# Performance work log

Hardware: AMD Instinct MI355X
Metric: run time of the kernel (lower is better)

## Reference

```python
import jax, jax.numpy as jnp
import numpy as np

D_MODEL = 128
N_HEADS = 8
N_POINTS = 8
MAX_RES = 10.0


def setup_inputs() -> dict:
    key = jax.random.key(0)
    ks = jax.random.split(key, 12)
    B, C, H, W = 4, D_MODEL, 128, 128
    nh, P = N_HEADS, N_POINTS
    inp = {
        'nbr_fea': jax.random.normal(ks[0], (B, C, H, W), jnp.float32),
        'ext_fea': jax.random.normal(ks[1], (B, C, H, W), jnp.float32),
        'flow': jax.random.normal(ks[2], (B, 2, H, W), jnp.float32) * 2.0,
        'W_off': jax.random.normal(ks[3], (C, nh * P * 2), jnp.float32) * 0.02,
        'b_off': jax.random.normal(ks[4], (nh * P * 2,), jnp.float32) * 0.02,
        'W_attn': jax.random.normal(ks[5], (C, nh * P), jnp.float32) * 0.02,
        'b_attn': jnp.zeros((nh * P,), jnp.float32),
        'W_val': jax.random.normal(ks[6], (C, C), jnp.float32) * (1.0 / np.sqrt(C)),
        'b_val': jnp.zeros((C,), jnp.float32),
        'W_out': jax.random.normal(ks[7], (C, C), jnp.float32) * (1.0 / np.sqrt(C)),
        'b_out': jnp.zeros((C,), jnp.float32),
    }
    return inp


def _bilinear_gather(value, loc, H, W):
    # value: (B, nh, HW, dh)  loc: (B, nh, Q, P, 2) normalized to [0,1]
    # grid_sample semantics: align_corners=False, zero padding
    B, nh, HW, dh = value.shape
    Q, P = loc.shape[2], loc.shape[3]
    x = loc[..., 0] * W - 0.5  # (B,nh,Q,P) pixel coords
    y = loc[..., 1] * H - 0.5
    x0 = jnp.floor(x)
    y0 = jnp.floor(y)
    wx = x - x0
    wy = y - y0
    out = jnp.zeros((B, nh, Q * P, dh), value.dtype)
    for dx, dy, wgt in ((0, 0, (1 - wx) * (1 - wy)), (1, 0, wx * (1 - wy)),
                        (0, 1, (1 - wx) * wy), (1, 1, wx * wy)):
        xi = x0 + dx
        yi = y0 + dy
        valid = (xi >= 0) & (xi < W) & (yi >= 0) & (yi < H)
        xi_c = jnp.clip(xi, 0, W - 1).astype(jnp.int32)
        yi_c = jnp.clip(yi, 0, H - 1).astype(jnp.int32)
        idx = (yi_c * W + xi_c).reshape(B, nh, Q * P, 1)
        g = jnp.take_along_axis(value, idx, axis=2)  # (B,nh,QP,dh)
        w_eff = (wgt * valid.astype(value.dtype)).reshape(B, nh, Q * P, 1)
        out = out + g * w_eff
    return out.reshape(B, nh, Q, P, dh)


def reference(nbr_fea, ext_fea, flow, W_off, b_off, W_attn, b_attn, W_val, b_val, W_out, b_out):
    B, C, H, W = nbr_fea.shape
    nh, P = N_HEADS, N_POINTS
    dh = C // nh
    Q = H * W
    # normalized reference points (pixel centers / extent)
    ys = (jnp.arange(H, dtype=jnp.float32) + 0.5) / H
    xs = (jnp.arange(W, dtype=jnp.float32) + 0.5) / W
    yy, xx = jnp.meshgrid(ys, xs, indexing='ij')
    ref = jnp.stack([xx, yy], -1).reshape(Q, 2)  # (Q,2)

    ext = ext_fea.transpose(0, 2, 3, 1).reshape(B, Q, C)
    # flow-guided sampling offsets (pixels), residue bounded by tanh
    off = MAX_RES * jnp.tanh(ext @ W_off + b_off)
    off = off.reshape(B, Q, nh, P, 2)
    flow_q = flow.transpose(0, 2, 3, 1).reshape(B, Q, 1, 1, 2)
    norm = jnp.array([W, H], jnp.float32)
    loc = ref[None, :, None, None, :] + (flow_q + off) / norm  # (B,Q,nh,P,2)

    attn = jax.nn.softmax((ext @ W_attn + b_attn).reshape(B, Q, nh, P), axis=-1)

    val = (nbr_fea.transpose(0, 2, 3, 1).reshape(B, Q, C) @ W_val + b_val)
    val = val.reshape(B, Q, nh, dh).transpose(0, 2, 1, 3)  # (B,nh,HW,dh)

    sampled = _bilinear_gather(val, loc.transpose(0, 2, 1, 3, 4), H, W)  # (B,nh,Q,P,dh)
    agg = jnp.einsum('bnqpd,bqnp->bqnd', sampled, attn).reshape(B, Q, C)
    out = agg @ W_out + b_out  # (B,Q,C)
    return out.reshape(B, H, W, C).transpose(0, 3, 1, 2)
```

## Files before the change

kernel.cpp:

```cpp
#include <hip/hip_runtime.h>
#include <math.h>

namespace {
constexpr int B   = 4;
constexpr int C   = 128;
constexpr int H   = 128;
constexpr int W   = 128;
constexpr int HWn = H * W;
constexpr int NH  = 8;
}

using short8 = __attribute__((ext_vector_type(8))) short;
using f32x4  = __attribute__((ext_vector_type(4))) float;

__device__ __forceinline__ float fast_tanh(float x) {
  float e = __expf(2.f * x);
  return 1.f - 2.f / (e + 1.f);
}
__device__ __forceinline__ unsigned f2bf(float f) {
  unsigned u = __float_as_uint(f);
  return (u + 0x7FFFu + ((u >> 16) & 1u)) >> 16;
}
__device__ __forceinline__ unsigned pack2bf(float a, float b) {
  return f2bf(a) | (f2bf(b) << 16);
}

__global__ __launch_bounds__(256) void prep_weights_kernel(
    const float* __restrict__ Woff, const float* __restrict__ Wattn,
    const float* __restrict__ Wval, const float* __restrict__ Wout,
    unsigned short* __restrict__ wcat_t, unsigned short* __restrict__ wval_t,
    unsigned short* __restrict__ wout_t) {
  int row = blockIdx.x * 256 + threadIdx.x;
  if (row >= 448) return;
  const float* src; int ldn; int col; unsigned short* dst;
  if (row < 192) {
    if (row < 128) { src = Woff; ldn = 128; col = row; }
    else           { src = Wattn; ldn = 64; col = row - 128; }
    dst = wcat_t + row * 128;
  } else if (row < 320) {
    src = Wval; ldn = 128; col = row - 192; dst = wval_t + (row - 192) * 128;
  } else {
    src = Wout; ldn = 128; col = row - 320; dst = wout_t + (row - 320) * 128;
  }
  for (int k0 = 0; k0 < 128; k0 += 8) {
    unsigned pk[4];
#pragma unroll
    for (int j = 0; j < 4; ++j)
      pk[j] = pack2bf(src[(k0 + 2 * j) * ldn + col],
                      src[(k0 + 2 * j + 1) * ldn + col]);
    *(uint4*)(dst + k0) = make_uint4(pk[0], pk[1], pk[2], pk[3]);
  }
}

__global__ __launch_bounds__(256) void val_gemm_kernel(
    const float* __restrict__ nbr, const unsigned short* __restrict__ wval_t,
    const float* __restrict__ bv, unsigned short* __restrict__ val) {
  __shared__ unsigned short a_s[64 * 152];
  __shared__ unsigned short b_s[128 * 40];
  const int t    = threadIdx.x;
  const int b    = blockIdx.x >> 8;
  const int q0   = (blockIdx.x & 255) * 64;
  const int wv   = t >> 6;
  const int lane = t & 63;
  const int li   = lane & 15, quad = lane >> 4;

  const float* Ab = nbr + (size_t)b * C * HWn + q0;
#pragma unroll
  for (int it = 0; it < 4; ++it) {
    int idx = t + 256 * it;
    int kp  = idx >> 4;
    int q4  = (idx & 15) * 4;
    float4 fa = *(const float4*)(Ab + (size_t)(2 * kp) * HWn + q4);
    float4 fb = *(const float4*)(Ab + (size_t)(2 * kp + 1) * HWn + q4);
    const float* pa = &fa.x; const float* pb = &fb.x;
#pragma unroll
    for (int j = 0; j < 4; ++j)
      *(unsigned*)&a_s[(q4 + j) * 152 + 2 * kp] = pack2bf(pa[j], pb[j]);
  }

  f32x4 acc[8];
#pragma unroll
  for (int n = 0; n < 8; ++n) acc[n] = (f32x4){0.f, 0.f, 0.f, 0.f};

  for (int ck = 0; ck < 4; ++ck) {
    __syncthreads();
#pragma unroll
    for (int it = 0; it < 2; ++it) {
      int idx = t + 256 * it;
      int n = idx >> 2, seg = idx & 3;
      *(uint4*)&b_s[n * 40 + seg * 8] =
          *(const uint4*)(wval_t + n * 128 + ck * 32 + seg * 8);
    }
    __syncthreads();
    short8 af = *(const short8*)&a_s[(16 * wv + li) * 152 + ck * 32 + quad * 8];
#pragma unroll
    for (int n = 0; n < 8; ++n) {
      short8 bfr = *(const short8*)&b_s[(16 * n + li) * 40 + quad * 8];
      acc[n] = __builtin_amdgcn_mfma_f32_16x16x32_bf16(af, bfr, acc[n], 0, 0, 0);
    }
  }

  __syncthreads();
#pragma unroll
  for (int n = 0; n < 8; ++n) {
    float bias = bv[16 * n + li];
#pragma unroll
    for (int reg = 0; reg < 4; ++reg) {
      int q = 16 * wv + 4 * quad + reg;
      a_s[q * 152 + 16 * n + li] = (unsigned short)f2bf(acc[n][reg] + bias);
    }
  }
  __syncthreads();
  {
    const int qi = t & 63, r = t >> 6;
    uint4 v0 = *(const uint4*)&a_s[qi * 152 + 32 * r];
    uint4 v1 = *(const uint4*)&a_s[qi * 152 + 32 * r + 8];
    uint4 v2 = *(const uint4*)&a_s[qi * 152 + 32 * r + 16];
    uint4 v3 = *(const uint4*)&a_s[qi * 152 + 32 * r + 24];
    unsigned short* d0 = val + ((size_t)(b * NH + 2 * r) * HWn + q0 + qi) * 16;
    unsigned short* d1 = val + ((size_t)(b * NH + 2 * r + 1) * HWn + q0 + qi) * 16;
    *(uint4*)d0 = v0; *(uint4*)(d0 + 8) = v1;
    *(uint4*)d1 = v2; *(uint4*)(d1 + 8) = v3;
  }
}

__global__ __launch_bounds__(256) void fused_kernel(
    const float* __restrict__ ext,  const float* __restrict__ flow,
    const unsigned short* __restrict__ wcat_t,
    const float* __restrict__ boff, const float* __restrict__ battn,
    const unsigned short* __restrict__ wout_t,
    const float* __restrict__ bout,
    const unsigned short* __restrict__ val, float* __restrict__ out) {
  __shared__ float smem[12352];
  const int t    = threadIdx.x;
  const int wv   = t >> 6;
  const int lane = t & 63;
  const int li   = lane & 15, quad = lane >> 4;
  const int qi   = t & 63;
  const int r    = t >> 6;

  const int blk  = blockIdx.x;
  const int lin  = (blk & 7) * 128 + (blk >> 3);
  const int b    = lin >> 8;
  const int tile = lin & 255;
  const int x0   = (tile & 7) * 16;
  const int y0   = (tile >> 3) * 4;
  const int x    = x0 + (qi & 15);
  const int y    = y0 + (qi >> 4);

  unsigned short* a_s  = (unsigned short*)smem;
  unsigned short* bw_s = (unsigned short*)(smem + 2560);
  f32x4 acc[12];
#pragma unroll
  for (int n = 0; n < 12; ++n) acc[n] = (f32x4){0.f, 0.f, 0.f, 0.f};

  const float* Eb = ext + (size_t)b * C * HWn;
  for (int ck = 0; ck < 4; ++ck) {
    const int k0 = ck * 32;
    __syncthreads();
    {
      int kp = t >> 4;
      int q4 = (t & 15) * 4;
      int yy = q4 >> 4, xx = q4 & 15;
      const float* srcp = Eb + (size_t)(k0 + 2 * kp) * HWn + (y0 + yy) * W + x0 + xx;
      float4 fa = *(const float4*)(srcp);
      float4 fb = *(const float4*)(srcp + HWn);
      const float* pa = &fa.x; const float* pb = &fb.x;
#pragma unroll
      for (int j = 0; j < 4; ++j) {
        unsigned ha = f2bf(pa[j]);
        unsigned hb = f2bf(pb[j]);
        float la = pa[j] - __uint_as_float(ha << 16);
        float lb = pb[j] - __uint_as_float(hb << 16);
        *(unsigned*)&a_s[(q4 + j) * 40 + 2 * kp]        = ha | (hb << 16);
        *(unsigned*)&a_s[2560 + (q4 + j) * 40 + 2 * kp] = pack2bf(la, lb);
      }
    }
#pragma unroll
    for (int it = 0; it < 3; ++it) {
      int idx = t + 256 * it;
      int n = idx >> 2, seg = idx & 3;
      *(uint4*)&bw_s[n * 40 + seg * 8] =
          *(const uint4*)(wcat_t + n * 128 + k0 + seg * 8);
    }
    __syncthreads();
    short8 ah = *(const short8*)&a_s[(16 * wv + li) * 40 + quad * 8];
    short8 al = *(const short8*)&a_s[2560 + (16 * wv + li) * 40 + quad * 8];
#pragma unroll
    for (int n = 0; n < 12; ++n) {
      short8 bfr = *(const short8*)&bw_s[(16 * n + li) * 40 + quad * 8];
      acc[n] = __builtin_amdgcn_mfma_f32_16x16x32_bf16(ah, bfr, acc[n], 0, 0, 0);
      acc[n] = __builtin_amdgcn_mfma_f32_16x16x32_bf16(al, bfr, acc[n], 0, 0, 0);
    }
  }

  __syncthreads();
#pragma unroll
  for (int n = 0; n < 12; ++n) {
    int col = 16 * n + li;
    float bias = (col < 128) ? boff[col] : battn[col - 128];
#pragma unroll
    for (int reg = 0; reg < 4; ++reg) {
      int q = 16 * wv + 4 * quad + reg;
      smem[q * 193 + col] = acc[n][reg] + bias;
    }
  }
  __syncthreads();

  float offa[32];
  float atta[16];
#pragma unroll
  for (int j = 0; j < 32; ++j)
    offa[j] = 10.f * fast_tanh(smem[qi * 193 + 32 * r + j]);
#pragma unroll
  for (int j = 0; j < 16; ++j) atta[j] = smem[qi * 193 + 128 + 16 * r + j];
#pragma unroll
  for (int u = 0; u < 2; ++u) {
    float* a = atta + 8 * u;
    float m = a[0];
#pragma unroll
    for (int p = 1; p < 8; ++p) m = fmaxf(m, a[p]);
    float s = 0.f;
#pragma unroll
    for (int p = 0; p < 8; ++p) { float ev = __expf(a[p] - m); a[p] = ev; s += ev; }
    float inv = 1.f / s;
#pragma unroll
    for (int p = 0; p < 8; ++p) a[p] *= inv;
  }

  const float xb = (float)x + flow[(size_t)b * 2 * HWn + y * W + x];
  const float yb = (float)y + flow[((size_t)b * 2 + 1) * HWn + y * W + x];

  float agg[32];
#pragma unroll
  for (int j = 0; j < 32; ++j) agg[j] = 0.f;
  const unsigned short* valb = val + (size_t)b * NH * HWn * 16;

#pragma unroll
  for (int u = 0; u < 2; ++u) {
    const unsigned short* valh = valb + (size_t)(2 * r + u) * HWn * 16;
    float* aggh = agg + 16 * u;
#pragma unroll
    for (int p = 0; p < 8; ++p) {
      float sx = xb + offa[u * 16 + 2 * p];
      float sy = yb + offa[u * 16 + 2 * p + 1];
      float x0f = floorf(sx), y0f = floorf(sy);
      float wx = sx - x0f, wy = sy - y0f;
      int ix0 = (int)x0f, iy0 = (int)y0f;
      int ix1 = ix0 + 1,  iy1 = iy0 + 1;
      float aw  = atta[u * 8 + p];
      float w00 = aw * (1.f - wx) * (1.f - wy);
      float w10 = aw * wx * (1.f - wy);
      float w01 = aw * (1.f - wx) * wy;
      float w11 = aw * wx * wy;
      if ((unsigned)ix0 >= (unsigned)W) { w00 = 0.f; w01 = 0.f; }
      if ((unsigned)ix1 >= (unsigned)W) { w10 = 0.f; w11 = 0.f; }
      if ((unsigned)iy0 >= (unsigned)H) { w00 = 0.f; w10 = 0.f; }
      if ((unsigned)iy1 >= (unsigned)H) { w01 = 0.f; w11 = 0.f; }
      int x0c = min(max(ix0, 0), W - 1);
      int x1c = min(max(ix1, 0), W - 1);
      int y0c = min(max(iy0, 0), H - 1);
      int y1c = min(max(iy1, 0), H - 1);
      const unsigned short* c00 = valh + (size_t)(y0c * W + x0c) * 16;
      const unsigned short* c10 = valh + (size_t)(y0c * W + x1c) * 16;
      const unsigned short* c01 = valh + (size_t)(y1c * W + x0c) * 16;
      const unsigned short* c11 = valh + (size_t)(y1c * W + x1c) * 16;
#pragma unroll
      for (int cn = 0; cn < 4; ++cn) {
        const unsigned short* cp = (cn == 0) ? c00 : (cn == 1) ? c10
                                  : (cn == 2) ? c01 : c11;
        float wgt = (cn == 0) ? w00 : (cn == 1) ? w10 : (cn == 2) ? w01 : w11;
        uint4 ga = ((const uint4*)cp)[0];
        uint4 gb = ((const uint4*)cp)[1];
        unsigned gs[8] = {ga.x, ga.y, ga.z, ga.w, gb.x, gb.y, gb.z, gb.w};
#pragma unroll
        for (int i = 0; i < 8; ++i) {
          float lo = __uint_as_float(gs[i] << 16);
          float hi = __uint_as_float(gs[i] & 0xFFFF0000u);
          aggh[2 * i]     += wgt * lo;
          aggh[2 * i + 1] += wgt * hi;
        }
      }
    }
  }

  __syncthreads();
  unsigned short* ag   = (unsigned short*)smem;
  unsigned short* w2_s = (unsigned short*)(smem + 4864);
  {
    unsigned pk[16];
#pragma unroll
    for (int i = 0; i < 16; ++i) pk[i] = pack2bf(agg[2 * i], agg[2 * i + 1]);
    uint4* dst = (uint4*)&ag[qi * 152 + 32 * r];
    dst[0] = make_uint4(pk[0],  pk[1],  pk[2],  pk[3]);
    dst[1] = make_uint4(pk[4],  pk[5],  pk[6],  pk[7]);
    dst[2] = make_uint4(pk[8],  pk[9],  pk[10], pk[11]);
    dst[3] = make_uint4(pk[12], pk[13], pk[14], pk[15]);
  }

  f32x4 acc2[8];
#pragma unroll
  for (int n = 0; n < 8; ++n) acc2[n] = (f32x4){0.f, 0.f, 0.f, 0.f};

  for (int ck = 0; ck < 4; ++ck) {
    __syncthreads();
#pragma unroll
    for (int it = 0; it < 2; ++it) {
      int idx = t + 256 * it;
      int n = idx >> 2, seg = idx & 3;
      *(uint4*)&w2_s[n * 40 + seg * 8] =
          *(const uint4*)(wout_t + n * 128 + ck * 32 + seg * 8);
    }
    __syncthreads();
    short8 af = *(const short8*)&ag[(16 * wv + li) * 152 + ck * 32 + quad * 8];
#pragma unroll
    for (int n = 0; n < 8; ++n) {
      short8 bfr = *(const short8*)&w2_s[(16 * n + li) * 40 + quad * 8];
      acc2[n] = __builtin_amdgcn_mfma_f32_16x16x32_bf16(af, bfr, acc2[n], 0, 0, 0);
    }
  }

  __syncthreads();
#pragma unroll
  for (int n = 0; n < 8; ++n) {
    float bias = bout[16 * n + li];
#pragma unroll
    for (int reg = 0; reg < 4; ++reg)
      smem[(16 * n + li) * 67 + 16 * wv + 4 * quad + reg] = acc2[n][reg] + bias;
  }
  __syncthreads();
  float* ob = out + (size_t)b * C * HWn + y * W + x;
#pragma unroll
  for (int j = 0; j < 32; ++j)
    ob[(size_t)(32 * r + j) * HWn] = smem[(32 * r + j) * 67 + qi];
}

extern "C" void kernel_launch(void* const* d_in, const int* in_sizes, int n_in,
                              void* d_out, int out_size, void* d_ws, size_t ws_size,
                              hipStream_t stream) {
  const float* nbr   = (const float*)d_in[0];
  const float* extf  = (const float*)d_in[1];
  const float* flow  = (const float*)d_in[2];
  const float* Woff  = (const float*)d_in[3];
  const float* boff  = (const float*)d_in[4];
  const float* Wattn = (const float*)d_in[5];
  const float* battn = (const float*)d_in[6];
  const float* Wval  = (const float*)d_in[7];
  const float* bval  = (const float*)d_in[8];
  const float* Wout  = (const float*)d_in[9];
  const float* bout  = (const float*)d_in[10];
  float* outp = (float*)d_out;

  unsigned short* val    = (unsigned short*)d_ws;
  unsigned short* wcat_t = val + (size_t)B * NH * HWn * 16;
  unsigned short* wval_t = wcat_t + 192 * 128;
  unsigned short* wout_t = wval_t + 128 * 128;

  prep_weights_kernel<<<dim3(2), dim3(256), 0, stream>>>(
      Woff, Wattn, Wval, Wout, wcat_t, wval_t, wout_t);
  val_gemm_kernel<<<dim3(1024), dim3(256), 0, stream>>>(
      nbr, wval_t, bval, val);
  fused_kernel<<<dim3(1024), dim3(256), 0, stream>>>(
      extf, flow, wcat_t, boff, battn, wout_t, bout, val, outp);
}
```

Baseline: 233.2 us.

## Halve fused kernel tile to 32 queries per block and one head per thread

The fused kernel now processes 32 query pixels per block instead of 64, launching 2048 blocks, with each thread handling one head instead of two. Per-thread register arrays and shared memory shrink, which should raise occupancy and the number of outstanding gathers. The offset/attention GEMM drops the hi/lo split-bf16 trick and uses a single bf16 pass, halving MFMAs at some accuracy cost. Output stores become float4 row writes, while weight tiles are now reloaded by twice as many blocks.

```diff
diff --git a/kernel.cpp b/kernel.cpp
--- a/kernel.cpp
+++ b/kernel.cpp
@@ -131,208 +131,206 @@
     const unsigned short* __restrict__ wout_t,
     const float* __restrict__ bout,
     const unsigned short* __restrict__ val, float* __restrict__ out) {
-  __shared__ float smem[12352];
+  __shared__ float smem[6176];
   const int t    = threadIdx.x;
   const int wv   = t >> 6;
   const int lane = t & 63;
   const int li   = lane & 15, quad = lane >> 4;
-  const int qi   = t & 63;
-  const int r    = t >> 6;
+  const int qi   = t & 31;
+  const int r    = t >> 5;
 
   const int blk  = blockIdx.x;
-  const int lin  = (blk & 7) * 128 + (blk >> 3);
-  const int b    = lin >> 8;
-  const int tile = lin & 255;
+  const int lin  = (blk & 7) * 256 + (blk >> 3);
+  const int b    = lin >> 9;
+  const int tile = lin & 511;
   const int x0   = (tile & 7) * 16;
-  const int y0   = (tile >> 3) * 4;
+  const int y0   = (tile >> 3) * 2;
   const int x    = x0 + (qi & 15);
   const int y    = y0 + (qi >> 4);
 
-  unsigned short* a_s  = (unsigned short*)smem;
-  unsigned short* bw_s = (unsigned short*)(smem + 2560);
-  f32x4 acc[12];
-#pragma unroll
-  for (int n = 0; n < 12; ++n) acc[n] = (f32x4){0.f, 0.f, 0.f, 0.f};
+  unsigned short* a_su = (unsigned short*)smem;
+  unsigned short* bw_s = (unsigned short*)smem + 1280;
+  const int mt = wv & 1;
+  const int nb = 6 * (wv >> 1);
+  f32x4 acc[6];
+#pragma unroll
+  for (int n = 0; n < 6; ++n) acc[n] = (f32x4){0.f, 0.f, 0.f, 0.f};
 
   const float* Eb = ext + (size_t)b * C * HWn;
   for (int ck = 0; ck < 4; ++ck) {
     const int k0 = ck * 32;
     __syncthreads();
-    {
-      int kp = t >> 4;
-      int q4 = (t & 15) * 4;
-      int yy = q4 >> 4, xx = q4 & 15;
-      const float* srcp = Eb + (size_t)(k0 + 2 * kp) * HWn + (y0 + yy) * W + x0 + xx;
+    if (t < 128) {
+      int kp = t >> 3, q4 = (t & 7) * 4;
+      int ay = q4 >> 4, ax = q4 & 15;
+      const float* srcp = Eb + (size_t)(k0 + 2 * kp) * HWn + (y0 + ay) * W + x0 + ax;
       float4 fa = *(const float4*)(srcp);
       float4 fb = *(const float4*)(srcp + HWn);
       const float* pa = &fa.x; const float* pb = &fb.x;
 #pragma unroll
-      for (int j = 0; j < 4; ++j) {
-        unsigned ha = f2bf(pa[j]);
-        unsigned hb = f2bf(pb[j]);
-        float la = pa[j] - __uint_as_float(ha << 16);
-        float lb = pb[j] - __uint_as_float(hb << 16);
-        *(unsigned*)&a_s[(q4 + j) * 40 + 2 * kp]        = ha | (hb << 16);
-        *(unsigned*)&a_s[2560 + (q4 + j) * 40 + 2 * kp] = pack2bf(la, lb);
+      for (int j = 0; j < 4; ++j)
+        *(unsigned*)&a_su[(q4 + j) * 40 + 2 * kp] = pack2bf(pa[j], pb[j]);
+    } else {
+      int tt = t - 128;
+#pragma unroll
+      for (int i = 0; i < 6; ++i) {
+        int idx = tt + 128 * i;
+        int n = idx >> 2, seg = idx & 3;
+        *(uint4*)&bw_s[n * 40 + seg * 8] =
+            *(const uint4*)(wcat_t + n * 128 + k0 + seg * 8);
       }
     }
-#pragma unroll
-    for (int it = 0; it < 3; ++it) {
-      int idx = t + 256 * it;
-      int n = idx >> 2, seg = idx & 3;
-      *(uint4*)&bw_s[n * 40 + seg * 8] =
-          *(const uint4*)(wcat_t + n * 128 + k0 + seg * 8);
-    }
-    __syncthreads();
-    short8 ah = *(const short8*)&a_s[(16 * wv + li) * 40 + quad * 8];
-    short8 al = *(const short8*)&a_s[2560 + (16 * wv + li) * 40 + quad * 8];
-#pragma unroll
-    for (int n = 0; n < 12; ++n) {
-      short8 bfr = *(const short8*)&bw_s[(16 * n + li) * 40 + quad * 8];
-      acc[n] = __builtin_amdgcn_mfma_f32_16x16x32_bf16(ah, bfr, acc[n], 0, 0, 0);
-      acc[n] = __builtin_amdgcn_mfma_f32_16x16x32_bf16(al, bfr, acc[n], 0, 0, 0);
-    }
-  }
-
-  __syncthreads();
-#pragma unroll
-  for (int n = 0; n < 12; ++n) {
-    int col = 16 * n + li;
+    __syncthreads();
+    short8 af = *(const short8*)&a_su[(16 * mt + li) * 40 + quad * 8];
+#pragma unroll
+    for (int n = 0; n < 6; ++n) {
+      short8 bfr = *(const short8*)&bw_s[(16 * (nb + n) + li) * 40 + quad * 8];
+      acc[n] = __builtin_amdgcn_mfma_f32_16x16x32_bf16(af, bfr, acc[n], 0, 0, 0);
+    }
+  }
+
+  __syncthreads();
+#pragma unroll
+  for (int n = 0; n < 6; ++n) {
+    int col = 16 * (nb + n) + li;
     float bias = (col < 128) ? boff[col] : battn[col - 128];
 #pragma unroll
     for (int reg = 0; reg < 4; ++reg) {
-      int q = 16 * wv + 4 * quad + reg;
+      int q = 16 * mt + 4 * quad + reg;
       smem[q * 193 + col] = acc[n][reg] + bias;
     }
   }
   __syncthreads();
 
-  float offa[32];
-  float atta[16];
-#pragma unroll
-  for (int j = 0; j < 32; ++j)
-    offa[j] = 10.f * fast_tanh(smem[qi * 193 + 32 * r + j]);
-#pragma unroll
-  for (int j = 0; j < 16; ++j) atta[j] = smem[qi * 193 + 128 + 16 * r + j];
-#pragma unroll
-  for (int u = 0; u < 2; ++u) {
-    float* a = atta + 8 * u;
-    float m = a[0];
-#pragma unroll
-    for (int p = 1; p < 8; ++p) m = fmaxf(m, a[p]);
+  float offa[16];
+  float atta[8];
+#pragma unroll
+  for (int j = 0; j < 16; ++j)
+    offa[j] = 10.f * fast_tanh(smem[qi * 193 + 16 * r + j]);
+#pragma unroll
+  for (int j = 0; j < 8; ++j) atta[j] = smem[qi * 193 + 128 + 8 * r + j];
+  {
+    float m = atta[0];
+#pragma unroll
+    for (int p = 1; p < 8; ++p) m = fmaxf(m, atta[p]);
     float s = 0.f;
 #pragma unroll
-    for (int p = 0; p < 8; ++p) { float ev = __expf(a[p] - m); a[p] = ev; s += ev; }
+    for (int p = 0; p < 8; ++p) { float ev = __expf(atta[p] - m); atta[p] = ev; s += ev; }
     float inv = 1.f / s;
 #pragma unroll
-    for (int p = 0; p < 8; ++p) a[p] *= inv;
-  }
+    for (int p = 0; p < 8; ++p) atta[p] *= inv;
+  }
+  __syncthreads();
 
   const float xb = (float)x + flow[(size_t)b * 2 * HWn + y * W + x];
   const float yb = (float)y + flow[((size_t)b * 2 + 1) * HWn + y * W + x];
 
-  float agg[32];
-#pragma unroll
-  for (int j = 0; j < 32; ++j) agg[j] = 0.f;
-  const unsigned short* valb = val + (size_t)b * NH * HWn * 16;
-
-#pragma unroll
-  for (int u = 0; u < 2; ++u) {
-    const unsigned short* valh = valb + (size_t)(2 * r + u) * HWn * 16;
-    float* aggh = agg + 16 * u;
-#pragma unroll
-    for (int p = 0; p < 8; ++p) {
-      float sx = xb + offa[u * 16 + 2 * p];
-      float sy = yb + offa[u * 16 + 2 * p + 1];
-      float x0f = floorf(sx), y0f = floorf(sy);
-      float wx = sx - x0f, wy = sy - y0f;
-      int ix0 = (int)x0f, iy0 = (int)y0f;
-      int ix1 = ix0 + 1,  iy1 = iy0 + 1;
-      float aw  = atta[u * 8 + p];
-      float w00 = aw * (1.f - wx) * (1.f - wy);
-      float w10 = aw * wx * (1.f - wy);
-      float w01 = aw * (1.f - wx) * wy;
-      float w11 = aw * wx * wy;
-      if ((unsigned)ix0 >= (unsigned)W) { w00 = 0.f; w01 = 0.f; }
-      if ((unsigned)ix1 >= (unsigned)W) { w10 = 0.f; w11 = 0.f; }
-      if ((unsigned)iy0 >= (unsigned)H) { w00 = 0.f; w10 = 0.f; }
-      if ((unsigned)iy1 >= (unsigned)H) { w01 = 0.f; w11 = 0.f; }
-      int x0c = min(max(ix0, 0), W - 1);
-      int x1c = min(max(ix1, 0), W - 1);
-      int y0c = min(max(iy0, 0), H - 1);
-      int y1c = min(max(iy1, 0), H - 1);
-      const unsigned short* c00 = valh + (size_t)(y0c * W + x0c) * 16;
-      const unsigned short* c10 = valh + (size_t)(y0c * W + x1c) * 16;
-      const unsigned short* c01 = valh + (size_t)(y1c * W + x0c) * 16;
-      const unsigned short* c11 = valh + (size_t)(y1c * W + x1c) * 16;
-#pragma unroll
-      for (int cn = 0; cn < 4; ++cn) {
-        const unsigned short* cp = (cn == 0) ? c00 : (cn == 1) ? c10
-                                  : (cn == 2) ? c01 : c11;
-        float wgt = (cn == 0) ? w00 : (cn == 1) ? w10 : (cn == 2) ? w01 : w11;
-        uint4 ga = ((const uint4*)cp)[0];
-        uint4 gb = ((const uint4*)cp)[1];
-        unsigned gs[8] = {ga.x, ga.y, ga.z, ga.w, gb.x, gb.y, gb.z, gb.w};
-#pragma unroll
-        for (int i = 0; i < 8; ++i) {
-          float lo = __uint_as_float(gs[i] << 16);
-          float hi = __uint_as_float(gs[i] & 0xFFFF0000u);
-          aggh[2 * i]     += wgt * lo;
-          aggh[2 * i + 1] += wgt * hi;
-        }
+  float agg[16];
+#pragma unroll
+  for (int j = 0; j < 16; ++j) agg[j] = 0.f;
+  const unsigned short* valh = val + (size_t)(b * NH + r) * HWn * 16;
+
+#pragma unroll
+  for (int p = 0; p < 8; ++p) {
+    float sx = xb + offa[2 * p];
+    float sy = yb + offa[2 * p + 1];
+    float x0f = floorf(sx), y0f = floorf(sy);
+    float wx = sx - x0f, wy = sy - y0f;
+    int ix0 = (int)x0f, iy0 = (int)y0f;
+    int ix1 = ix0 + 1,  iy1 = iy0 + 1;
+    float aw  = atta[p];
+    float w00 = aw * (1.f - wx) * (1.f - wy);
+    float w10 = aw * wx * (1.f - wy);
+    float w01 = aw * (1.f - wx) * wy;
+    float w11 = aw * wx * wy;
+    if ((unsigned)ix0 >= (unsigned)W) { w00 = 0.f; w01 = 0.f; }
+    if ((unsigned)ix1 >= (unsigned)W) { w10 = 0.f; w11 = 0.f; }
+    if ((unsigned)iy0 >= (unsigned)H) { w00 = 0.f; w10 = 0.f; }
+    if ((unsigned)iy1 >= (unsigned)H) { w01 = 0.f; w11 = 0.f; }
+    int x0c = min(max(ix0, 0), W - 1);
+    int x1c = min(max(ix1, 0), W - 1);
+    int y0c = min(max(iy0, 0), H - 1);
+    int y1c = min(max(iy1, 0), H - 1);
+    const unsigned short* c00 = valh + (size_t)(y0c * W + x0c) * 16;
+    const unsigned short* c10 = valh + (size_t)(y0c * W + x1c) * 16;
+    const unsigned short* c01 = valh + (size_t)(y1c * W + x0c) * 16;
+    const unsigned short* c11 = valh + (size_t)(y1c * W + x1c) * 16;
+#pragma unroll
+    for (int cn = 0; cn < 4; ++cn) {
+      const unsigned short* cp = (cn == 0) ? c00 : (cn == 1) ? c10
+                                : (cn == 2) ? c01 : c11;
+      float wgt = (cn == 0) ? w00 : (cn == 1) ? w10 : (cn == 2) ? w01 : w11;
+      uint4 ga = ((const uint4*)cp)[0];
+      uint4 gb = ((const uint4*)cp)[1];
+      unsigned gs[8] = {ga.x, ga.y, ga.z, ga.w, gb.x, gb.y, gb.z, gb.w};
+#pragma unroll
+      for (int i = 0; i < 8; ++i) {
+        float lo = __uint_as_float(gs[i] << 16);
+        float hi = __uint_as_float(gs[i] & 0xFFFF0000u);
+        agg[2 * i]     += wgt * lo;
+        agg[2 * i + 1] += wgt * hi;
       }
     }
   }
 
-  __syncthreads();
   unsigned short* ag   = (unsigned short*)smem;
-  unsigned short* w2_s = (unsigned short*)(smem + 4864);
+  unsigned short* w2_s = (unsigned short*)smem + 2 * 2176;
   {
-    unsigned pk[16];
-#pragma unroll
-    for (int i = 0; i < 16; ++i) pk[i] = pack2bf(agg[2 * i], agg[2 * i + 1]);
-    uint4* dst = (uint4*)&ag[qi * 152 + 32 * r];
-    dst[0] = make_uint4(pk[0],  pk[1],  pk[2],  pk[3]);
-    dst[1] = make_uint4(pk[4],  pk[5],  pk[6],  pk[7]);
-    dst[2] = make_uint4(pk[8],  pk[9],  pk[10], pk[11]);
-    dst[3] = make_uint4(pk[12], pk[13], pk[14], pk[15]);
-  }
-
-  f32x4 acc2[8];
-#pragma unroll
-  for (int n = 0; n < 8; ++n) acc2[n] = (f32x4){0.f, 0.f, 0.f, 0.f};
+    unsigned pk[8];
+#pragma unroll
+    for (int i = 0; i < 8; ++i) pk[i] = pack2bf(agg[2 * i], agg[2 * i + 1]);
+    uint4* dst = (uint4*)&ag[qi * 136 + 16 * r];
+    dst[0] = make_uint4(pk[0], pk[1], pk[2], pk[3]);
+    dst[1] = make_uint4(pk[4], pk[5], pk[6], pk[7]);
+  }
+
+  const int nb2 = 4 * (wv >> 1);
+  f32x4 acc2[4];
+#pragma unroll
+  for (int n = 0; n < 4; ++n) acc2[n] = (f32x4){0.f, 0.f, 0.f, 0.f};
 
   for (int ck = 0; ck < 4; ++ck) {
     __syncthreads();
 #pragma unroll
-    for (int it = 0; it < 2; ++it) {
-      int idx = t + 256 * it;
+    for (int i = 0; i < 2; ++i) {
+      int idx = t + 256 * i;
       int n = idx >> 2, seg = idx & 3;
       *(uint4*)&w2_s[n * 40 + seg * 8] =
           *(const uint4*)(wout_t + n * 128 + ck * 32 + seg * 8);
     }
     __syncthreads();
-    short8 af = *(const short8*)&ag[(16 * wv + li) * 152 + ck * 32 + quad * 8];
-#pragma unroll
-    for (int n = 0; n < 8; ++n) {
-      short8 bfr = *(const short8*)&w2_s[(16 * n + li) * 40 + quad * 8];
-      acc2[n] = __builtin_amdgcn_mfma_f32_16x16x32_bf16(af, bfr, acc2[n], 0, 0, 0);
-    }
-  }
-
-  __syncthreads();
-#pragma unroll
-  for (int n = 0; n < 8; ++n) {
-    float bias = bout[16 * n + li];
+    short8 af2 = *(const short8*)&ag[(16 * mt + li) * 136 + ck * 32 + quad * 8];
+#pragma unroll
+    for (int n = 0; n < 4; ++n) {
+      short8 bfr = *(const short8*)&w2_s[(16 * (nb2 + n) + li) * 40 + quad * 8];
+      acc2[n] = __builtin_amdgcn_mfma_f32_16x16x32_bf16(af2, bfr, acc2[n], 0, 0, 0);
+    }
+  }
+
+  __syncthreads();
+#pragma unroll
+  for (int n = 0; n < 4; ++n) {
+    int c = 16 * (nb2 + n) + li;
+    float bias = bout[c];
 #pragma unroll
     for (int reg = 0; reg < 4; ++reg)
-      smem[(16 * n + li) * 67 + 16 * wv + 4 * quad + reg] = acc2[n][reg] + bias;
-  }
-  __syncthreads();
-  float* ob = out + (size_t)b * C * HWn + y * W + x;
-#pragma unroll
-  for (int j = 0; j < 32; ++j)
-    ob[(size_t)(32 * r + j) * HWn] = smem[(32 * r + j) * 67 + qi];
+      smem[c * 37 + 16 * mt + 4 * quad + reg] = acc2[n][reg] + bias;
+  }
+  __syncthreads();
+  {
+    const int c  = t >> 1;
+    const int yy = t & 1;
+    float* orow = out + (size_t)b * C * HWn + (size_t)c * HWn + (y0 + yy) * W + x0;
+#pragma unroll
+    for (int s = 0; s < 4; ++s) {
+      float4 v;
+      v.x = smem[c * 37 + yy * 16 + 4 * s + 0];
+      v.y = smem[c * 37 + yy * 16 + 4 * s + 1];
+      v.z = smem[c * 37 + yy * 16 + 4 * s + 2];
+      v.w = smem[c * 37 + yy * 16 + 4 * s + 3];
+      *(float4*)(orow + 4 * s) = v;
+    }
+  }
 }
 
 extern "C" void kernel_launch(void* const* d_in, const int* in_sizes, int n_in,
@@ -360,6 +358,6 @@
       Woff, Wattn, Wval, Wout, wcat_t, wval_t, wout_t);
   val_gemm_kernel<<<dim3(1024), dim3(256), 0, stream>>>(
       nbr, wval_t, bval, val);
-  fused_kernel<<<dim3(1024), dim3(256), 0, stream>>>(
+  fused_kernel<<<dim3(2048), dim3(256), 0, stream>>>(
       extf, flow, wcat_t, boff, battn, wout_t, bout, val, outp);
 }
```

Result: slower. 258.9 us (+11.0%).

## Move offset/attention projection into shared GEMM kernel, use FP32 output projection

Applied to the files above, without the earlier changes.

The ext-feature offset/attention projection moves out of the fused kernel into a combined GEMM launch (2048 blocks: value projection plus projection of ext), written to an fp32 proj buffer in workspace. The bf16 hi/lo split for that projection is dropped, so it uses single bf16 MFMA (lower precision for offsets). The output projection in the gather kernel is replaced with FP32 scalar FMA from LDS-staged fp32 Wout instead of bf16 MFMA. The aim is better parallelism and occupancy, at the cost of extra global traffic for proj (~50MB) and much more ALU work for the output GEMM.

```diff
diff --git a/kernel.cpp b/kernel.cpp
--- a/kernel.cpp
+++ b/kernel.cpp
@@ -8,6 +8,7 @@
 constexpr int W   = 128;
 constexpr int HWn = H * W;
 constexpr int NH  = 8;
+constexpr int KC  = 16;
 }
 
 using short8 = __attribute__((ext_vector_type(8))) short;
@@ -27,20 +28,17 @@
 
 __global__ __launch_bounds__(256) void prep_weights_kernel(
     const float* __restrict__ Woff, const float* __restrict__ Wattn,
-    const float* __restrict__ Wval, const float* __restrict__ Wout,
-    unsigned short* __restrict__ wcat_t, unsigned short* __restrict__ wval_t,
-    unsigned short* __restrict__ wout_t) {
+    const float* __restrict__ Wval,
+    unsigned short* __restrict__ wcat_t, unsigned short* __restrict__ wval_t) {
   int row = blockIdx.x * 256 + threadIdx.x;
-  if (row >= 448) return;
+  if (row >= 320) return;
   const float* src; int ldn; int col; unsigned short* dst;
   if (row < 192) {
     if (row < 128) { src = Woff; ldn = 128; col = row; }
     else           { src = Wattn; ldn = 64; col = row - 128; }
     dst = wcat_t + row * 128;
-  } else if (row < 320) {
+  } else {
     src = Wval; ldn = 128; col = row - 192; dst = wval_t + (row - 192) * 128;
-  } else {
-    src = Wout; ldn = 128; col = row - 320; dst = wout_t + (row - 320) * 128;
   }
   for (int k0 = 0; k0 < 128; k0 += 8) {
     unsigned pk[4];
@@ -52,19 +50,25 @@
   }
 }
 
-__global__ __launch_bounds__(256) void val_gemm_kernel(
-    const float* __restrict__ nbr, const unsigned short* __restrict__ wval_t,
-    const float* __restrict__ bv, unsigned short* __restrict__ val) {
+__global__ __launch_bounds__(256) void gemm_kernel(
+    const float* __restrict__ nbr, const float* __restrict__ ext,
+    const unsigned short* __restrict__ wval_t,
+    const float* __restrict__ bv,
+    const unsigned short* __restrict__ wcat_t,
+    const float* __restrict__ boff, const float* __restrict__ battn,
+    unsigned short* __restrict__ val, float* __restrict__ proj) {
   __shared__ unsigned short a_s[64 * 152];
-  __shared__ unsigned short b_s[128 * 40];
+  __shared__ unsigned short b_s[192 * 40];
   const int t    = threadIdx.x;
-  const int b    = blockIdx.x >> 8;
-  const int q0   = (blockIdx.x & 255) * 64;
+  const int grp  = blockIdx.x >> 10;
+  const int id   = blockIdx.x & 1023;
+  const int b    = id >> 8;
+  const int q0   = (id & 255) * 64;
   const int wv   = t >> 6;
   const int lane = t & 63;
   const int li   = lane & 15, quad = lane >> 4;
 
-  const float* Ab = nbr + (size_t)b * C * HWn + q0;
+  const float* Ab = (grp ? ext : nbr) + (size_t)b * C * HWn + q0;
 #pragma unroll
   for (int it = 0; it < 4; ++it) {
     int idx = t + 256 * it;
@@ -78,66 +82,97 @@
       *(unsigned*)&a_s[(q4 + j) * 152 + 2 * kp] = pack2bf(pa[j], pb[j]);
   }
 
-  f32x4 acc[8];
-#pragma unroll
-  for (int n = 0; n < 8; ++n) acc[n] = (f32x4){0.f, 0.f, 0.f, 0.f};
-
-  for (int ck = 0; ck < 4; ++ck) {
+  if (grp == 0) {
+    f32x4 acc[8];
+#pragma unroll
+    for (int n = 0; n < 8; ++n) acc[n] = (f32x4){0.f, 0.f, 0.f, 0.f};
+
+    for (int ck = 0; ck < 4; ++ck) {
+      __syncthreads();
+#pragma unroll
+      for (int it = 0; it < 2; ++it) {
+        int idx = t + 256 * it;
+        int n = idx >> 2, seg = idx & 3;
+        *(uint4*)&b_s[n * 40 + seg * 8] =
+            *(const uint4*)(wval_t + n * 128 + ck * 32 + seg * 8);
+      }
+      __syncthreads();
+      short8 af = *(const short8*)&a_s[(16 * wv + li) * 152 + ck * 32 + quad * 8];
+#pragma unroll
+      for (int n = 0; n < 8; ++n) {
+        short8 bfr = *(const short8*)&b_s[(16 * n + li) * 40 + quad * 8];
+        acc[n] = __builtin_amdgcn_mfma_f32_16x16x32_bf16(af, bfr, acc[n], 0, 0, 0);
+      }
+    }
+
     __syncthreads();
 #pragma unroll
-    for (int it = 0; it < 2; ++it) {
-      int idx = t + 256 * it;
-      int n = idx >> 2, seg = idx & 3;
-      *(uint4*)&b_s[n * 40 + seg * 8] =
-          *(const uint4*)(wval_t + n * 128 + ck * 32 + seg * 8);
+    for (int n = 0; n < 8; ++n) {
+      float bias = bv[16 * n + li];
+#pragma unroll
+      for (int reg = 0; reg < 4; ++reg) {
+        int q = 16 * wv + 4 * quad + reg;
+        a_s[q * 152 + 16 * n + li] = (unsigned short)f2bf(acc[n][reg] + bias);
+      }
     }
     __syncthreads();
-    short8 af = *(const short8*)&a_s[(16 * wv + li) * 152 + ck * 32 + quad * 8];
-#pragma unroll
-    for (int n = 0; n < 8; ++n) {
-      short8 bfr = *(const short8*)&b_s[(16 * n + li) * 40 + quad * 8];
-      acc[n] = __builtin_amdgcn_mfma_f32_16x16x32_bf16(af, bfr, acc[n], 0, 0, 0);
-    }
-  }
-
-  __syncthreads();
-#pragma unroll
-  for (int n = 0; n < 8; ++n) {
-    float bias = bv[16 * n + li];
-#pragma unroll
-    for (int reg = 0; reg < 4; ++reg) {
-      int q = 16 * wv + 4 * quad + reg;
-      a_s[q * 152 + 16 * n + li] = (unsigned short)f2bf(acc[n][reg] + bias);
-    }
-  }
-  __syncthreads();
-  {
-    const int qi = t & 63, r = t >> 6;
-    uint4 v0 = *(const uint4*)&a_s[qi * 152 + 32 * r];
-    uint4 v1 = *(const uint4*)&a_s[qi * 152 + 32 * r + 8];
-    uint4 v2 = *(const uint4*)&a_s[qi * 152 + 32 * r + 16];
-    uint4 v3 = *(const uint4*)&a_s[qi * 152 + 32 * r + 24];
-    unsigned short* d0 = val + ((size_t)(b * NH + 2 * r) * HWn + q0 + qi) * 16;
-    unsigned short* d1 = val + ((size_t)(b * NH + 2 * r + 1) * HWn + q0 + qi) * 16;
-    *(uint4*)d0 = v0; *(uint4*)(d0 + 8) = v1;
-    *(uint4*)d1 = v2; *(uint4*)(d1 + 8) = v3;
-  }
-}
-
-__global__ __launch_bounds__(256) void fused_kernel(
-    const float* __restrict__ ext,  const float* __restrict__ flow,
-    const unsigned short* __restrict__ wcat_t,
-    const float* __restrict__ boff, const float* __restrict__ battn,
-    const unsigned short* __restrict__ wout_t,
-    const float* __restrict__ bout,
-    const unsigned short* __restrict__ val, float* __restrict__ out) {
-  __shared__ float smem[12352];
-  const int t    = threadIdx.x;
-  const int wv   = t >> 6;
-  const int lane = t & 63;
-  const int li   = lane & 15, quad = lane >> 4;
-  const int qi   = t & 63;
-  const int r    = t >> 6;
+    {
+      const int qi = t & 63, r = t >> 6;
+      uint4 v0 = *(const uint4*)&a_s[qi * 152 + 32 * r];
+      uint4 v1 = *(const uint4*)&a_s[qi * 152 + 32 * r + 8];
+      uint4 v2 = *(const uint4*)&a_s[qi * 152 + 32 * r + 16];
+      uint4 v3 = *(const uint4*)&a_s[qi * 152 + 32 * r + 24];
+      unsigned short* d0 = val + ((size_t)(b * NH + 2 * r) * HWn + q0 + qi) * 16;
+      unsigned short* d1 = val + ((size_t)(b * NH + 2 * r + 1) * HWn + q0 + qi) * 16;
+      *(uint4*)d0 = v0; *(uint4*)(d0 + 8) = v1;
+      *(uint4*)d1 = v2; *(uint4*)(d1 + 8) = v3;
+    }
+  } else {
+    f32x4 acc[12];
+#pragma unroll
+    for (int n = 0; n < 12; ++n) acc[n] = (f32x4){0.f, 0.f, 0.f, 0.f};
+
+    for (int ck = 0; ck < 4; ++ck) {
+      __syncthreads();
+#pragma unroll
+      for (int it = 0; it < 3; ++it) {
+        int idx = t + 256 * it;
+        int n = idx >> 2, seg = idx & 3;
+        *(uint4*)&b_s[n * 40 + seg * 8] =
+            *(const uint4*)(wcat_t + n * 128 + ck * 32 + seg * 8);
+      }
+      __syncthreads();
+      short8 af = *(const short8*)&a_s[(16 * wv + li) * 152 + ck * 32 + quad * 8];
+#pragma unroll
+      for (int n = 0; n < 12; ++n) {
+        short8 bfr = *(const short8*)&b_s[(16 * n + li) * 40 + quad * 8];
+        acc[n] = __builtin_amdgcn_mfma_f32_16x16x32_bf16(af, bfr, acc[n], 0, 0, 0);
+      }
+    }
+
+#pragma unroll
+    for (int n = 0; n < 12; ++n) {
+      int col = 16 * n + li;
+      float bias = (col < 128) ? boff[col] : battn[col - 128];
+#pragma unroll
+      for (int reg = 0; reg < 4; ++reg) {
+        int q = 16 * wv + 4 * quad + reg;
+        proj[(size_t)(b * HWn + q0 + q) * 192 + col] = acc[n][reg] + bias;
+      }
+    }
+  }
+}
+
+__global__ __launch_bounds__(256) void gather_out_kernel(
+    const float* __restrict__ flow, const float* __restrict__ proj,
+    const unsigned short* __restrict__ val,
+    const float* __restrict__ Wout, const float* __restrict__ bout,
+    float* __restrict__ out) {
+  __shared__ float agg_s[C * 64];
+  __shared__ float w_s[KC * 128];
+  const int t  = threadIdx.x;
+  const int qi = t & 63;
+  const int r  = t >> 6;
 
   const int blk  = blockIdx.x;
   const int lin  = (blk & 7) * 128 + (blk >> 3);
@@ -148,72 +183,23 @@
   const int x    = x0 + (qi & 15);
   const int y    = y0 + (qi >> 4);
 
-  unsigned short* a_s  = (unsigned short*)smem;
-  unsigned short* bw_s = (unsigned short*)(smem + 2560);
-  f32x4 acc[12];
-#pragma unroll
-  for (int n = 0; n < 12; ++n) acc[n] = (f32x4){0.f, 0.f, 0.f, 0.f};
-
-  const float* Eb = ext + (size_t)b * C * HWn;
-  for (int ck = 0; ck < 4; ++ck) {
-    const int k0 = ck * 32;
-    __syncthreads();
-    {
-      int kp = t >> 4;
-      int q4 = (t & 15) * 4;
-      int yy = q4 >> 4, xx = q4 & 15;
-      const float* srcp = Eb + (size_t)(k0 + 2 * kp) * HWn + (y0 + yy) * W + x0 + xx;
-      float4 fa = *(const float4*)(srcp);
-      float4 fb = *(const float4*)(srcp + HWn);
-      const float* pa = &fa.x; const float* pb = &fb.x;
-#pragma unroll
-      for (int j = 0; j < 4; ++j) {
-        unsigned ha = f2bf(pa[j]);
-        unsigned hb = f2bf(pb[j]);
-        float la = pa[j] - __uint_as_float(ha << 16);
-        float lb = pb[j] - __uint_as_float(hb << 16);
-        *(unsigned*)&a_s[(q4 + j) * 40 + 2 * kp]        = ha | (hb << 16);
-        *(unsigned*)&a_s[2560 + (q4 + j) * 40 + 2 * kp] = pack2bf(la, lb);
-      }
-    }
-#pragma unroll
-    for (int it = 0; it < 3; ++it) {
-      int idx = t + 256 * it;
-      int n = idx >> 2, seg = idx & 3;
-      *(uint4*)&bw_s[n * 40 + seg * 8] =
-          *(const uint4*)(wcat_t + n * 128 + k0 + seg * 8);
-    }
-    __syncthreads();
-    short8 ah = *(const short8*)&a_s[(16 * wv + li) * 40 + quad * 8];
-    short8 al = *(const short8*)&a_s[2560 + (16 * wv + li) * 40 + quad * 8];
-#pragma unroll
-    for (int n = 0; n < 12; ++n) {
-      short8 bfr = *(const short8*)&bw_s[(16 * n + li) * 40 + quad * 8];
-      acc[n] = __builtin_amdgcn_mfma_f32_16x16x32_bf16(ah, bfr, acc[n], 0, 0, 0);
-      acc[n] = __builtin_amdgcn_mfma_f32_16x16x32_bf16(al, bfr, acc[n], 0, 0, 0);
-    }
-  }
-
-  __syncthreads();
-#pragma unroll
-  for (int n = 0; n < 12; ++n) {
-    int col = 16 * n + li;
-    float bias = (col < 128) ? boff[col] : battn[col - 128];
-#pragma unroll
-    for (int reg = 0; reg < 4; ++reg) {
-      int q = 16 * wv + 4 * quad + reg;
-      smem[q * 193 + col] = acc[n][reg] + bias;
-    }
-  }
-  __syncthreads();
-
+  const float* pp = proj + (size_t)(b * HWn + y * W + x) * 192;
   float offa[32];
   float atta[16];
 #pragma unroll
-  for (int j = 0; j < 32; ++j)
-    offa[j] = 10.f * fast_tanh(smem[qi * 193 + 32 * r + j]);
-#pragma unroll
-  for (int j = 0; j < 16; ++j) atta[j] = smem[qi * 193 + 128 + 16 * r + j];
+  for (int j4 = 0; j4 < 8; ++j4) {
+    float4 v = *(const float4*)(pp + 32 * r + 4 * j4);
+    offa[4 * j4 + 0] = 10.f * fast_tanh(v.x);
+    offa[4 * j4 + 1] = 10.f * fast_tanh(v.y);
+    offa[4 * j4 + 2] = 10.f * fast_tanh(v.z);
+    offa[4 * j4 + 3] = 10.f * fast_tanh(v.w);
+  }
+#pragma unroll
+  for (int j4 = 0; j4 < 4; ++j4) {
+    float4 v = *(const float4*)(pp + 128 + 16 * r + 4 * j4);
+    atta[4 * j4 + 0] = v.x; atta[4 * j4 + 1] = v.y;
+    atta[4 * j4 + 2] = v.z; atta[4 * j4 + 3] = v.w;
+  }
 #pragma unroll
   for (int u = 0; u < 2; ++u) {
     float* a = atta + 8 * u;
@@ -284,55 +270,41 @@
     }
   }
 
-  __syncthreads();
-  unsigned short* ag   = (unsigned short*)smem;
-  unsigned short* w2_s = (unsigned short*)(smem + 4864);
-  {
-    unsigned pk[16];
-#pragma unroll
-    for (int i = 0; i < 16; ++i) pk[i] = pack2bf(agg[2 * i], agg[2 * i + 1]);
-    uint4* dst = (uint4*)&ag[qi * 152 + 32 * r];
-    dst[0] = make_uint4(pk[0],  pk[1],  pk[2],  pk[3]);
-    dst[1] = make_uint4(pk[4],  pk[5],  pk[6],  pk[7]);
-    dst[2] = make_uint4(pk[8],  pk[9],  pk[10], pk[11]);
-    dst[3] = make_uint4(pk[12], pk[13], pk[14], pk[15]);
-  }
-
-  f32x4 acc2[8];
-#pragma unroll
-  for (int n = 0; n < 8; ++n) acc2[n] = (f32x4){0.f, 0.f, 0.f, 0.f};
-
-  for (int ck = 0; ck < 4; ++ck) {
+#pragma unroll
+  for (int j = 0; j < 32; ++j) agg_s[(32 * r + j) * 64 + qi] = agg[j];
+
+  float acc[32];
+#pragma unroll
+  for (int j = 0; j < 32; ++j) acc[j] = bout[32 * r + j];
+
+  for (int ck = 0; ck < C / KC; ++ck) {
+    const int k0 = ck * KC;
+#pragma unroll
+    for (int i = 0; i < 2; ++i) {
+      int idx = t + 256 * i;
+      int k = idx >> 5, col = (idx & 31) * 4;
+      *(float4*)&w_s[k * 128 + col] =
+          *(const float4*)(Wout + (size_t)(k0 + k) * 128 + col);
+    }
     __syncthreads();
 #pragma unroll
-    for (int it = 0; it < 2; ++it) {
-      int idx = t + 256 * it;
-      int n = idx >> 2, seg = idx & 3;
-      *(uint4*)&w2_s[n * 40 + seg * 8] =
-          *(const uint4*)(wout_t + n * 128 + ck * 32 + seg * 8);
+    for (int k = 0; k < KC; ++k) {
+      float a = agg_s[(k0 + k) * 64 + qi];
+      const float4* wp = (const float4*)&w_s[k * 128 + 32 * r];
+#pragma unroll
+      for (int j4 = 0; j4 < 8; ++j4) {
+        float4 w = wp[j4];
+        acc[4 * j4 + 0] += a * w.x; acc[4 * j4 + 1] += a * w.y;
+        acc[4 * j4 + 2] += a * w.z; acc[4 * j4 + 3] += a * w.w;
+      }
     }
     __syncthreads();
-    short8 af = *(const short8*)&ag[(16 * wv + li) * 152 + ck * 32 + quad * 8];
-#pragma unroll
-    for (int n = 0; n < 8; ++n) {
-      short8 bfr = *(const short8*)&w2_s[(16 * n + li) * 40 + quad * 8];
-      acc2[n] = __builtin_amdgcn_mfma_f32_16x16x32_bf16(af, bfr, acc2[n], 0, 0, 0);
-    }
-  }
-
-  __syncthreads();
-#pragma unroll
-  for (int n = 0; n < 8; ++n) {
-    float bias = bout[16 * n + li];
-#pragma unroll
-    for (int reg = 0; reg < 4; ++reg)
-      smem[(16 * n + li) * 67 + 16 * wv + 4 * quad + reg] = acc2[n][reg] + bias;
-  }
-  __syncthreads();
+  }
+
   float* ob = out + (size_t)b * C * HWn + y * W + x;
 #pragma unroll
   for (int j = 0; j < 32; ++j)
-    ob[(size_t)(32 * r + j) * HWn] = smem[(32 * r + j) * 67 + qi];
+    ob[(size_t)(32 * r + j) * HWn] = acc[j];
 }
 
 extern "C" void kernel_launch(void* const* d_in, const int* in_sizes, int n_in,
@@ -354,12 +326,12 @@
   unsigned short* val    = (unsigned short*)d_ws;
   unsigned short* wcat_t = val + (size_t)B * NH * HWn * 16;
   unsigned short* wval_t = wcat_t + 192 * 128;
-  unsigned short* wout_t = wval_t + 128 * 128;
+  float*          proj   = (float*)(wval_t + 128 * 128);
 
   prep_weights_kernel<<<dim3(2), dim3(256), 0, stream>>>(
-      Woff, Wattn, Wval, Wout, wcat_t, wval_t, wout_t);
-  val_gemm_kernel<<<dim3(1024), dim3(256), 0, stream>>>(
-      nbr, wval_t, bval, val);
-  fused_kernel<<<dim3(1024), dim3(256), 0, stream>>>(
-      extf, flow, wcat_t, boff, battn, wout_t, bout, val, outp);
-}
+      Woff, Wattn, Wval, wcat_t, wval_t);
+  gemm_kernel<<<dim3(2048), dim3(256), 0, stream>>>(
+      nbr, extf, wval_t, bval, wcat_t, boff, battn, val, proj);
+  gather_out_kernel<<<dim3(1024), dim3(256), 0, stream>>>(
+      flow, proj, val, Wout, bout, outp);
+}
```

Result: no change. 231.8 us (-0.6%).
